# Performance work log

Measured on AMD Instinct MI355X. Metric: run time of the kernel, lower is better.

The kernel has to match this reference:

```python
import jax, jax.numpy as jnp
import numpy as np

N_NODES = 20000   # original graph nodes
E_G = 200000      # original graph edges = line-graph nodes
E_LG = 2000000    # line-graph edges
D_IN = 64
D_H = 128


def setup_inputs() -> dict:
    key = jax.random.key(0)
    ks = jax.random.split(key, 9)
    x = jax.random.normal(ks[0], (N_NODES, D_IN), dtype=jnp.float32)
    g_edge_index = jax.random.randint(ks[1], (2, E_G), 0, N_NODES)
    lg_edge_index = jax.random.randint(ks[2], (2, E_LG), 0, E_G)
    s = 0.05
    W0 = jax.random.normal(ks[3], (2 * D_IN, D_H), dtype=jnp.float32) * s
    b0 = jnp.zeros((D_H,), dtype=jnp.float32)
    W1 = jax.random.normal(ks[4], (D_H, D_H), dtype=jnp.float32) * s
    b1 = jnp.zeros((D_H,), dtype=jnp.float32)
    Wl = jax.random.normal(ks[5], (D_H, 1), dtype=jnp.float32) * s
    bl = jnp.zeros((1,), dtype=jnp.float32)
    return {"x": x, "g_edge_index": g_edge_index, "lg_edge_index": lg_edge_index,
            "index01": 0, "W0": W0, "b0": b0, "W1": W1, "b1": b1, "Wl": Wl, "bl": bl}


def gcn_conv(h, edge_index, W, b, n):
    # PyG GCNConv: add self-loops, symmetric deg^{-1/2} normalization,
    # linear transform then gather-scale-scatter aggregation, then bias.
    loop = jnp.arange(n)
    row = jnp.concatenate([edge_index[0], loop])  # source j
    col = jnp.concatenate([edge_index[1], loop])  # target i
    deg = jax.ops.segment_sum(jnp.ones(row.shape, h.dtype), col, num_segments=n)
    dinv = jnp.where(deg > 0, jax.lax.rsqrt(deg), 0.0)
    norm = dinv[row] * dinv[col]                   # [E+n]
    hw = h @ W                                     # [n, D_out]
    msg = hw[row] * norm[:, None]                  # gather + scale
    out = jax.ops.segment_sum(msg, col, num_segments=n)  # scatter-add
    return out + b


def reference(x, g_edge_index, lg_edge_index, index01, W0, b0, W1, b1, Wl, bl):
    # to_line_graph_features: concat endpoint features per original edge
    h = jnp.concatenate([x[g_edge_index[0]], x[g_edge_index[1]]], axis=-1)  # [E_G, 2*D_IN]
    n = h.shape[0]
    h = jax.nn.relu(gcn_conv(h, lg_edge_index, W0, b0, n))
    h = jax.nn.relu(gcn_conv(h, lg_edge_index, W1, b1, n))
    sel = h[index01][None, :]                      # [1, D_H]
    return jax.nn.sigmoid(sel @ Wl + bl)           # [1, 1]
```

## Files before the change

kernel.cpp:

```cpp
#include <hip/hip_runtime.h>
#include <math.h>

#define MAX_L1 512
#define MAX_S2 (MAX_L1 + 8)
#define MAX_L2 4096
#define MAX_S3 (MAX_L2 + MAX_S2 + 8)
#define SCAN_BLOCKS 2048
#define HW0_BLOCKS 64

enum { CNT_L1 = 0, CNT_S2 = 1, CNT_L2 = 2, CNT_S3 = 3 };

__device__ __forceinline__ void insert_s3(int n, unsigned* bits3, int* cnt,
                                          int* s3_list, int* slot) {
  unsigned m = 1u << (n & 31);
  if (!(atomicOr(&bits3[n >> 5], m) & m)) {
    int p = atomicAdd(&cnt[CNT_S3], 1);
    if (p < MAX_S3) { s3_list[p] = n; slot[n] = p; }
  }
}

__device__ __forceinline__ void insert_s2(int n, unsigned* bits2, int* cnt,
                                          int* s2_list, int* s2pos,
                                          unsigned* bits3, int* s3_list,
                                          int* slot) {
  unsigned m = 1u << (n & 31);
  if (!(atomicOr(&bits2[n >> 5], m) & m)) {
    int p = atomicAdd(&cnt[CNT_S2], 1);
    if (p < MAX_S2) { s2_list[p] = n; s2pos[n] = p; }
  }
  insert_s3(n, bits3, cnt, s3_list, slot);
}

__global__ void __launch_bounds__(256) k_scan1(
    const int* __restrict__ lg, int e_lg, const int* __restrict__ pidx,
    int* __restrict__ cnt, unsigned* __restrict__ bits2,
    unsigned* __restrict__ bits3, int* __restrict__ list1,
    int* __restrict__ s2_list, int* __restrict__ s2pos,
    int* __restrict__ s3_list, int* __restrict__ slot) {
  const int idx0 = pidx[0];
  const int gtid = blockIdx.x * blockDim.x + threadIdx.x;
  const int gstride = gridDim.x * blockDim.x;
  if (gtid == 0) insert_s2(idx0, bits2, cnt, s2_list, s2pos, bits3, s3_list, slot);
  const int* __restrict__ col = lg + e_lg;
  const int n4 = ((((uintptr_t)col) & 15) == 0) ? (e_lg >> 2) : 0;
  const int4* __restrict__ col4 = (const int4*)col;
  for (int i = gtid; i < n4; i += gstride) {
    int4 v = col4[i];
    int cc[4] = {v.x, v.y, v.z, v.w};
#pragma unroll
    for (int k = 0; k < 4; ++k) {
      if (cc[k] == idx0) {
        int r = lg[i * 4 + k];
        int p = atomicAdd(&cnt[CNT_L1], 1);
        if (p < MAX_L1) list1[p] = r;
        insert_s2(r, bits2, cnt, s2_list, s2pos, bits3, s3_list, slot);
      }
    }
  }
  for (int e = n4 * 4 + gtid; e < e_lg; e += gstride) {
    if (col[e] == idx0) {
      int r = lg[e];
      int p = atomicAdd(&cnt[CNT_L1], 1);
      if (p < MAX_L1) list1[p] = r;
      insert_s2(r, bits2, cnt, s2_list, s2pos, bits3, s3_list, slot);
    }
  }
}

__global__ void __launch_bounds__(256) k_scan2(
    const int* __restrict__ lg, int e_lg, int* __restrict__ cnt,
    const unsigned* __restrict__ bits2, unsigned* __restrict__ bits3,
    int2* __restrict__ list2, int* __restrict__ s3_list,
    int* __restrict__ slot) {
  const int gtid = blockIdx.x * blockDim.x + threadIdx.x;
  const int gstride = gridDim.x * blockDim.x;
  const int* __restrict__ col = lg + e_lg;
  const int n4 = ((((uintptr_t)col) & 15) == 0) ? (e_lg >> 2) : 0;
  const int4* __restrict__ col4 = (const int4*)col;
  for (int i = gtid; i < n4; i += gstride) {
    int4 v = col4[i];
    int cc[4] = {v.x, v.y, v.z, v.w};
#pragma unroll
    for (int k = 0; k < 4; ++k) {
      int c = cc[k];
      if ((bits2[c >> 5] >> (c & 31)) & 1u) {
        int r = lg[i * 4 + k];
        int p = atomicAdd(&cnt[CNT_L2], 1);
        if (p < MAX_L2) list2[p] = make_int2(r, c);
        insert_s3(r, bits3, cnt, s3_list, slot);
      }
    }
  }
  for (int e = n4 * 4 + gtid; e < e_lg; e += gstride) {
    int c = col[e];
    if ((bits2[c >> 5] >> (c & 31)) & 1u) {
      int r = lg[e];
      int p = atomicAdd(&cnt[CNT_L2], 1);
      if (p < MAX_L2) list2[p] = make_int2(r, c);
      insert_s3(r, bits3, cnt, s3_list, slot);
    }
  }
}

__global__ void __launch_bounds__(256) k_deg_hw0(
    const int* __restrict__ lg, int e_lg, const float* __restrict__ x,
    const int* __restrict__ g, int e_g, const float* __restrict__ W0,
    const int* __restrict__ cnt, const unsigned* __restrict__ bits3,
    const int* __restrict__ slot, int* __restrict__ degc,
    const int* __restrict__ s3_list, float* __restrict__ hw0) {
  const int tid = threadIdx.x;
  if (blockIdx.x < gridDim.x - HW0_BLOCKS) {
    const int gtid = blockIdx.x * blockDim.x + tid;
    const int gstride = (gridDim.x - HW0_BLOCKS) * blockDim.x;
    const int* __restrict__ col = lg + e_lg;
    const int n4 = ((((uintptr_t)col) & 15) == 0) ? (e_lg >> 2) : 0;
    const int4* __restrict__ col4 = (const int4*)col;
    for (int i = gtid; i < n4; i += gstride) {
      int4 v = col4[i];
      int cc[4] = {v.x, v.y, v.z, v.w};
#pragma unroll
      for (int k = 0; k < 4; ++k) {
        int c = cc[k];
        if ((bits3[c >> 5] >> (c & 31)) & 1u) atomicAdd(&degc[slot[c]], 1);
      }
    }
    for (int e = n4 * 4 + gtid; e < e_lg; e += gstride) {
      int c = col[e];
      if ((bits3[c >> 5] >> (c & 31)) & 1u) atomicAdd(&degc[slot[c]], 1);
    }
  } else {
    int ns3 = min(cnt[CNT_S3], MAX_S3);
    int hb = (blockIdx.x - (gridDim.x - HW0_BLOCKS)) * 2 + (tid >> 7);
    int t = tid & 127;
    for (int b = hb; b < ns3; b += HW0_BLOCKS * 2) {
      int node = s3_list[b];
      int src = g[node];
      int dst = g[e_g + node];
      float acc = 0.f;
#pragma unroll 8
      for (int k = 0; k < 64; ++k) acc += x[src * 64 + k] * W0[k * 128 + t];
#pragma unroll 8
      for (int k = 0; k < 64; ++k) acc += x[dst * 64 + k] * W0[(64 + k) * 128 + t];
      hw0[b * 128 + t] = acc;
    }
  }
}

__global__ void __launch_bounds__(256) k_h1_hw1(
    const int* __restrict__ cnt, const int* __restrict__ s2_list,
    const int* __restrict__ slot, const int* __restrict__ degc,
    const int2* __restrict__ list2, const float* __restrict__ hw0,
    const float* __restrict__ b0, const float* __restrict__ W1,
    float* __restrict__ hw1) {
  int ns2 = min(cnt[CNT_S2], MAX_S2);
  if ((int)blockIdx.x >= ns2) return;
  int j = s2_list[blockIdx.x];
  int t = threadIdx.x & 127;
  int grp = threadIdx.x >> 7;
  __shared__ float part[2][128];
  __shared__ float h1s[128];
  float dj = rsqrtf((float)degc[slot[j]] + 1.0f);
  float acc = (grp == 0) ? hw0[slot[j] * 128 + t] * dj * dj + b0[t] : 0.f;
  int n2 = min(cnt[CNT_L2], MAX_L2);
  for (int i = grp; i < n2; i += 2) {
    int2 e = list2[i];
    if (e.y == j) {
      float dr = rsqrtf((float)degc[slot[e.x]] + 1.0f);
      acc += hw0[slot[e.x] * 128 + t] * (dr * dj);
    }
  }
  part[grp][t] = acc;
  __syncthreads();
  if (grp == 0) h1s[t] = fmaxf(part[0][t] + part[1][t], 0.f);
  __syncthreads();
  float a2 = 0.f;
  int k0 = grp * 64;
#pragma unroll 8
  for (int k = 0; k < 64; ++k) a2 += h1s[k0 + k] * W1[(k0 + k) * 128 + t];
  part[grp][t] = a2;
  __syncthreads();
  if (grp == 0) hw1[blockIdx.x * 128 + t] = part[0][t] + part[1][t];
}

__global__ void __launch_bounds__(128) k_final(
    const int* __restrict__ cnt, const int* __restrict__ pidx,
    const int* __restrict__ list1, const int* __restrict__ s2pos,
    const int* __restrict__ slot, const int* __restrict__ degc,
    const float* __restrict__ hw1, const float* __restrict__ b1,
    const float* __restrict__ Wl, const float* __restrict__ bl,
    float* __restrict__ out) {
  int t = threadIdx.x;
  int idx0 = pidx[0];
  float d0 = rsqrtf((float)degc[slot[idx0]] + 1.0f);
  float acc = hw1[s2pos[idx0] * 128 + t] * d0 * d0;
  int n1 = min(cnt[CNT_L1], MAX_L1);
  for (int i = 0; i < n1; ++i) {
    int r = list1[i];
    float dr = rsqrtf((float)degc[slot[r]] + 1.0f);
    acc += hw1[s2pos[r] * 128 + t] * (dr * d0);
  }
  float h2 = fmaxf(acc + b1[t], 0.f);
  __shared__ float red[128];
  red[t] = h2 * Wl[t];
  __syncthreads();
  for (int s = 64; s > 0; s >>= 1) {
    if (t < s) red[t] += red[t + s];
    __syncthreads();
  }
  if (t == 0) out[0] = 1.f / (1.f + expf(-(red[0] + bl[0])));
}

extern "C" void kernel_launch(void* const* d_in, const int* in_sizes, int n_in,
                              void* d_out, int out_size, void* d_ws, size_t ws_size,
                              hipStream_t stream) {
  const float* x  = (const float*)d_in[0];
  const int* g    = (const int*)d_in[1];
  const int* lg   = (const int*)d_in[2];
  const int* pidx = (const int*)d_in[3];
  const float* W0 = (const float*)d_in[4];
  const float* b0 = (const float*)d_in[5];
  const float* W1 = (const float*)d_in[6];
  const float* b1 = (const float*)d_in[7];
  const float* Wl = (const float*)d_in[8];
  const float* bl = (const float*)d_in[9];
  float* out = (float*)d_out;

  int e_g = in_sizes[1] / 2;
  int e_lg = in_sizes[2] / 2;

  char* ws = (char*)d_ws;
  size_t off = 0;
  auto take = [&](size_t bytes) {
    size_t cur = off;
    off = (off + bytes + 15) & ~(size_t)15;
    return cur;
  };
  const size_t nbits_words = ((size_t)e_g + 31) / 32;
  int* cnt        = (int*)(ws + take(16 * 4));
  unsigned* bits2 = (unsigned*)(ws + take(nbits_words * 4));
  unsigned* bits3 = (unsigned*)(ws + take(nbits_words * 4));
  int* degc       = (int*)(ws + take((size_t)MAX_S3 * 4));
  size_t zero_bytes = off;
  int* list1      = (int*)(ws + take(MAX_L1 * 4));
  int* s2_list    = (int*)(ws + take(MAX_S2 * 4));
  int* s2pos      = (int*)(ws + take((size_t)e_g * 4));
  int2* list2     = (int2*)(ws + take((size_t)MAX_L2 * 8));
  int* s3_list    = (int*)(ws + take((size_t)MAX_S3 * 4));
  int* slot       = (int*)(ws + take((size_t)e_g * 4));
  float* hw0      = (float*)(ws + take((size_t)MAX_S3 * 128 * 4));
  float* hw1      = (float*)(ws + take((size_t)MAX_S2 * 128 * 4));
  (void)ws_size;

  hipMemsetAsync(d_ws, 0, zero_bytes, stream);

  k_scan1<<<SCAN_BLOCKS, 256, 0, stream>>>(lg, e_lg, pidx, cnt, bits2, bits3,
                                           list1, s2_list, s2pos, s3_list, slot);
  k_scan2<<<SCAN_BLOCKS, 256, 0, stream>>>(lg, e_lg, cnt, bits2, bits3, list2,
                                           s3_list, slot);
  k_deg_hw0<<<SCAN_BLOCKS + HW0_BLOCKS, 256, 0, stream>>>(
      lg, e_lg, x, g, e_g, W0, cnt, bits3, slot, degc, s3_list, hw0);
  k_h1_hw1<<<MAX_S2, 256, 0, stream>>>(cnt, s2_list, slot, degc, list2, hw0, b0,
                                       W1, hw1);
  k_final<<<1, 128, 0, stream>>>(cnt, pidx, list1, s2pos, slot, degc, hw1, b1,
                                 Wl, bl, out);
}
```

Before: 148.2 us.

## Fuse h1/hw1 and final stages into last-block tail of degree kernel

Merges the layer-1 aggregation/hw1 kernel and the final readout kernel into the degree/hw0 kernel, run by the last block to finish through an atomic ticket. It also halves the scan grid size. The aim is to remove two kernel launches and their gaps. The cost is that all ns2 (up to ~520) hw1 rows, each scanning list2 serially, are now computed by a single block rather than hundreds of blocks in parallel.

```diff
diff --git a/kernel.cpp b/kernel.cpp
--- a/kernel.cpp
+++ b/kernel.cpp
@@ -5,10 +5,10 @@
 #define MAX_S2 (MAX_L1 + 8)
 #define MAX_L2 4096
 #define MAX_S3 (MAX_L2 + MAX_S2 + 8)
-#define SCAN_BLOCKS 2048
-#define HW0_BLOCKS 64
-
-enum { CNT_L1 = 0, CNT_S2 = 1, CNT_L2 = 2, CNT_S3 = 3 };
+#define SCAN_B 1024
+#define HW0_B 64
+
+enum { CNT_L1 = 0, CNT_S2 = 1, CNT_L2 = 2, CNT_S3 = 3, CNT_TICKET = 4 };
 
 __device__ __forceinline__ void insert_s3(int n, unsigned* bits3, int* cnt,
                                           int* s3_list, int* slot) {
@@ -102,16 +102,22 @@
   }
 }
 
-__global__ void __launch_bounds__(256) k_deg_hw0(
+__global__ void __launch_bounds__(256) k_deg_hw0_tail(
     const int* __restrict__ lg, int e_lg, const float* __restrict__ x,
     const int* __restrict__ g, int e_g, const float* __restrict__ W0,
-    const int* __restrict__ cnt, const unsigned* __restrict__ bits3,
+    const float* __restrict__ b0, const float* __restrict__ W1,
+    const float* __restrict__ b1, const float* __restrict__ Wl,
+    const float* __restrict__ bl, const int* __restrict__ pidx,
+    int* __restrict__ cnt, const unsigned* __restrict__ bits3,
     const int* __restrict__ slot, int* __restrict__ degc,
-    const int* __restrict__ s3_list, float* __restrict__ hw0) {
+    const int* __restrict__ s3_list, const int* __restrict__ s2_list,
+    const int* __restrict__ s2pos, const int* __restrict__ list1,
+    const int2* __restrict__ list2, float* __restrict__ hw0,
+    float* __restrict__ hw1, float* __restrict__ out) {
   const int tid = threadIdx.x;
-  if (blockIdx.x < gridDim.x - HW0_BLOCKS) {
+  if (blockIdx.x < SCAN_B) {
     const int gtid = blockIdx.x * blockDim.x + tid;
-    const int gstride = (gridDim.x - HW0_BLOCKS) * blockDim.x;
+    const int gstride = SCAN_B * blockDim.x;
     const int* __restrict__ col = lg + e_lg;
     const int n4 = ((((uintptr_t)col) & 15) == 0) ? (e_lg >> 2) : 0;
     const int4* __restrict__ col4 = (const int4*)col;
@@ -130,9 +136,9 @@
     }
   } else {
     int ns3 = min(cnt[CNT_S3], MAX_S3);
-    int hb = (blockIdx.x - (gridDim.x - HW0_BLOCKS)) * 2 + (tid >> 7);
+    int hb = (blockIdx.x - SCAN_B) * 2 + (tid >> 7);
     int t = tid & 127;
-    for (int b = hb; b < ns3; b += HW0_BLOCKS * 2) {
+    for (int b = hb; b < ns3; b += HW0_B * 2) {
       int node = s3_list[b];
       int src = g[node];
       int dst = g[e_g + node];
@@ -144,70 +150,69 @@
       hw0[b * 128 + t] = acc;
     }
   }
-}
-
-__global__ void __launch_bounds__(256) k_h1_hw1(
-    const int* __restrict__ cnt, const int* __restrict__ s2_list,
-    const int* __restrict__ slot, const int* __restrict__ degc,
-    const int2* __restrict__ list2, const float* __restrict__ hw0,
-    const float* __restrict__ b0, const float* __restrict__ W1,
-    float* __restrict__ hw1) {
+
+  __threadfence();
+  __shared__ int is_last;
+  if (tid == 0) {
+    int done = atomicAdd(&cnt[CNT_TICKET], 1);
+    is_last = (done == (int)gridDim.x - 1);
+  }
+  __syncthreads();
+  if (!is_last) return;
+  __threadfence();
+
   int ns2 = min(cnt[CNT_S2], MAX_S2);
-  if ((int)blockIdx.x >= ns2) return;
-  int j = s2_list[blockIdx.x];
-  int t = threadIdx.x & 127;
-  int grp = threadIdx.x >> 7;
+  int n2 = min(cnt[CNT_L2], MAX_L2);
+  int t = tid & 127;
+  int grp = tid >> 7;
   __shared__ float part[2][128];
   __shared__ float h1s[128];
-  float dj = rsqrtf((float)degc[slot[j]] + 1.0f);
-  float acc = (grp == 0) ? hw0[slot[j] * 128 + t] * dj * dj + b0[t] : 0.f;
-  int n2 = min(cnt[CNT_L2], MAX_L2);
-  for (int i = grp; i < n2; i += 2) {
-    int2 e = list2[i];
-    if (e.y == j) {
-      float dr = rsqrtf((float)degc[slot[e.x]] + 1.0f);
-      acc += hw0[slot[e.x] * 128 + t] * (dr * dj);
-    }
-  }
-  part[grp][t] = acc;
+  for (int b = 0; b < ns2; ++b) {
+    int j = s2_list[b];
+    float dj = rsqrtf((float)degc[slot[j]] + 1.0f);
+    float acc = (grp == 0) ? hw0[slot[j] * 128 + t] * dj * dj + b0[t] : 0.f;
+    for (int i = grp; i < n2; i += 2) {
+      int2 e = list2[i];
+      if (e.y == j) {
+        float dr = rsqrtf((float)degc[slot[e.x]] + 1.0f);
+        acc += hw0[slot[e.x] * 128 + t] * (dr * dj);
+      }
+    }
+    part[grp][t] = acc;
+    __syncthreads();
+    if (grp == 0) h1s[t] = fmaxf(part[0][t] + part[1][t], 0.f);
+    __syncthreads();
+    float a2 = 0.f;
+    int k0 = grp * 64;
+#pragma unroll 8
+    for (int k = 0; k < 64; ++k) a2 += h1s[k0 + k] * W1[(k0 + k) * 128 + t];
+    part[grp][t] = a2;
+    __syncthreads();
+    if (grp == 0) hw1[b * 128 + t] = part[0][t] + part[1][t];
+    __syncthreads();
+  }
+
+  if (grp == 0) {
+    int idx0 = pidx[0];
+    float d0 = rsqrtf((float)degc[slot[idx0]] + 1.0f);
+    float acc = hw1[s2pos[idx0] * 128 + t] * d0 * d0;
+    int n1 = min(cnt[CNT_L1], MAX_L1);
+    for (int i = 0; i < n1; ++i) {
+      int r = list1[i];
+      float dr = rsqrtf((float)degc[slot[r]] + 1.0f);
+      acc += hw1[s2pos[r] * 128 + t] * (dr * d0);
+    }
+    float h2 = fmaxf(acc + b1[t], 0.f);
+    h1s[t] = h2 * Wl[t];
+  }
   __syncthreads();
-  if (grp == 0) h1s[t] = fmaxf(part[0][t] + part[1][t], 0.f);
-  __syncthreads();
-  float a2 = 0.f;
-  int k0 = grp * 64;
-#pragma unroll 8
-  for (int k = 0; k < 64; ++k) a2 += h1s[k0 + k] * W1[(k0 + k) * 128 + t];
-  part[grp][t] = a2;
-  __syncthreads();
-  if (grp == 0) hw1[blockIdx.x * 128 + t] = part[0][t] + part[1][t];
-}
-
-__global__ void __launch_bounds__(128) k_final(
-    const int* __restrict__ cnt, const int* __restrict__ pidx,
-    const int* __restrict__ list1, const int* __restrict__ s2pos,
-    const int* __restrict__ slot, const int* __restrict__ degc,
-    const float* __restrict__ hw1, const float* __restrict__ b1,
-    const float* __restrict__ Wl, const float* __restrict__ bl,
-    float* __restrict__ out) {
-  int t = threadIdx.x;
-  int idx0 = pidx[0];
-  float d0 = rsqrtf((float)degc[slot[idx0]] + 1.0f);
-  float acc = hw1[s2pos[idx0] * 128 + t] * d0 * d0;
-  int n1 = min(cnt[CNT_L1], MAX_L1);
-  for (int i = 0; i < n1; ++i) {
-    int r = list1[i];
-    float dr = rsqrtf((float)degc[slot[r]] + 1.0f);
-    acc += hw1[s2pos[r] * 128 + t] * (dr * d0);
-  }
-  float h2 = fmaxf(acc + b1[t], 0.f);
-  __shared__ float red[128];
-  red[t] = h2 * Wl[t];
-  __syncthreads();
-  for (int s = 64; s > 0; s >>= 1) {
-    if (t < s) red[t] += red[t + s];
-    __syncthreads();
-  }
-  if (t == 0) out[0] = 1.f / (1.f + expf(-(red[0] + bl[0])));
+  if (grp == 0) {
+    for (int s = 64; s > 0; s >>= 1) {
+      if (t < s) h1s[t] += h1s[t + s];
+      __syncthreads();
+    }
+    if (t == 0) out[0] = 1.f / (1.f + expf(-(h1s[0] + bl[0])));
+  }
 }
 
 extern "C" void kernel_launch(void* const* d_in, const int* in_sizes, int n_in,
@@ -253,14 +258,11 @@
 
   hipMemsetAsync(d_ws, 0, zero_bytes, stream);
 
-  k_scan1<<<SCAN_BLOCKS, 256, 0, stream>>>(lg, e_lg, pidx, cnt, bits2, bits3,
-                                           list1, s2_list, s2pos, s3_list, slot);
-  k_scan2<<<SCAN_BLOCKS, 256, 0, stream>>>(lg, e_lg, cnt, bits2, bits3, list2,
-                                           s3_list, slot);
-  k_deg_hw0<<<SCAN_BLOCKS + HW0_BLOCKS, 256, 0, stream>>>(
-      lg, e_lg, x, g, e_g, W0, cnt, bits3, slot, degc, s3_list, hw0);
-  k_h1_hw1<<<MAX_S2, 256, 0, stream>>>(cnt, s2_list, slot, degc, list2, hw0, b0,
-                                       W1, hw1);
-  k_final<<<1, 128, 0, stream>>>(cnt, pidx, list1, s2pos, slot, degc, hw1, b1,
-                                 Wl, bl, out);
-}
+  k_scan1<<<SCAN_B, 256, 0, stream>>>(lg, e_lg, pidx, cnt, bits2, bits3,
+                                      list1, s2_list, s2pos, s3_list, slot);
+  k_scan2<<<SCAN_B, 256, 0, stream>>>(lg, e_lg, cnt, bits2, bits3, list2,
+                                      s3_list, slot);
+  k_deg_hw0_tail<<<SCAN_B + HW0_B, 256, 0, stream>>>(
+      lg, e_lg, x, g, e_g, W0, b0, W1, b1, Wl, bl, pidx, cnt, bits3, slot,
+      degc, s3_list, s2_list, s2pos, list1, list2, hw0, hw1, out);
+}
```

Result: slower. 435.0 us (+193.5%).
